# Kernel tuning notes

Hardware: AMD Instinct MI355X
Metric: run time of the kernel (lower is better)

The kernel has to match this reference:

```python
import jax, jax.numpy as jnp
import numpy as np

EMBED_DIM = 768
NUM_HEADS = 12
HEAD_DIM = EMBED_DIM // NUM_HEADS


def setup_inputs() -> dict:
    key = jax.random.key(0)
    k_x, k_wqkv, k_bqkv, k_wp, k_bp = jax.random.split(key, 5)
    B, S, D = 4, 2048, EMBED_DIM
    # nn.Linear default init scale ~ 1/sqrt(fan_in); exact distribution irrelevant for a reference
    lim = 1.0 / np.sqrt(D)
    x = jax.random.normal(k_x, (B, S, D), dtype=jnp.float32)
    w_qkv = jax.random.uniform(k_wqkv, (D, 3 * D), jnp.float32, -lim, lim)
    b_qkv = jax.random.uniform(k_bqkv, (3 * D,), jnp.float32, -lim, lim)
    w_proj = jax.random.uniform(k_wp, (D, D), jnp.float32, -lim, lim)
    b_proj = jax.random.uniform(k_bp, (D,), jnp.float32, -lim, lim)
    return {"x": x, "w_qkv": w_qkv, "b_qkv": b_qkv, "w_proj": w_proj, "b_proj": b_proj}


def reference(x, w_qkv, b_qkv, w_proj, b_proj):
    B, S, D = x.shape
    H, Hd = NUM_HEADS, HEAD_DIM
    qkv = x @ w_qkv + b_qkv                      # [B,S,3D]
    qkv = qkv.reshape(B, S, 3, H, Hd)
    qkv = jnp.transpose(qkv, (2, 0, 3, 1, 4))     # [3,B,H,S,Hd]
    q, k, v = qkv[0], qkv[1], qkv[2]
    scale = 1.0 / np.sqrt(Hd).astype(np.float32)
    scores = jnp.einsum("bhsd,bhtd->bhst", q, k) * scale  # [B,H,S,S]
    attn = jax.nn.softmax(scores, axis=-1)
    out = jnp.einsum("bhst,bhtd->bhsd", attn, v)  # [B,H,S,Hd]
    out = jnp.transpose(out, (0, 2, 1, 3)).reshape(B, S, D)
    return out @ w_proj + b_proj
```

## Files before the change

### kernel.cpp

```cpp
#include <hip/hip_runtime.h>


typedef _Float16 f16;
typedef _Float16 f16x8 __attribute__((ext_vector_type(8)));
typedef _Float16 f16x4 __attribute__((ext_vector_type(4)));
typedef float f32x4 __attribute__((ext_vector_type(4)));

#define BQ 4
#define SQ 2048
#define DQ 768
#define HQ 12
#define HD 64
#define M_TOK (BQ*SQ)
#define KVB 64
#define QSCALE 0.18033688f
#define THR_LOG2 11.5f

__device__ __forceinline__ void gld_lds16(const f16* g, f16* l) {
  __builtin_amdgcn_global_load_lds((const __attribute__((address_space(1))) void*)g,
                                   (__attribute__((address_space(3))) void*)l,
                                   16, 0, 0);
}

__global__ __launch_bounds__(256)
void prep(const float* __restrict__ x, f16* __restrict__ xh,
          const float* __restrict__ w_qkv, f16* __restrict__ wqkvT,
          const float* __restrict__ w_proj, f16* __restrict__ wprojT)
{
  __shared__ float tile[32][33];
  const int bid = blockIdx.x, tid = threadIdx.x;
  if (bid < 6144) {
    int i = (bid * 256 + tid) * 4;
    float4 v = *(const float4*)(x + i);
    f16x4 o = { (f16)v.x, (f16)v.y, (f16)v.z, (f16)v.w };
    *(f16x4*)(xh + i) = o;
    return;
  }
  const float* w; f16* wt; int K, N, nb, kb;
  if (bid < 7872) {
    int b2 = bid - 6144; w = w_qkv; wt = wqkvT; K = DQ; N = 3 * DQ;
    nb = (b2 % 72) * 32; kb = (b2 / 72) * 32;
  } else {
    int b3 = bid - 7872; w = w_proj; wt = wprojT; K = DQ; N = DQ;
    nb = (b3 % 24) * 32; kb = (b3 / 24) * 32;
  }
  int tx = tid & 31, ty = tid >> 5;
  for (int r = ty; r < 32; r += 8)
    tile[r][tx] = w[(size_t)(kb + r) * N + nb + tx];
  __syncthreads();
  for (int r = ty; r < 32; r += 8)
    wt[(size_t)(nb + r) * K + kb + tx] = (f16)tile[tx][r];
}

template<int MODE>
__global__ __launch_bounds__(256, 2)
void gemm128(const f16* __restrict__ A, const f16* __restrict__ Bt,
             const float* __restrict__ bias, float* __restrict__ Cf,
             f16* __restrict__ Qb, f16* __restrict__ Kb, f16* __restrict__ Vt,
             int M, int N, int K, int nbx)
{
  __shared__ f16 Ash[2][128 * 32];
  __shared__ f16 Bsh[2][128 * 32];
  const int tid = threadIdx.x;
  const int bid = blockIdx.x;
  const int nb = bid % nbx, mb = bid / nbx;
  const int m0 = mb * 128, n0 = nb * 128;
  const int lane = tid & 63, wid = tid >> 6;
  const int wr = wid >> 1, wc = wid & 1;
  const int l16 = lane & 15, l4 = lane >> 4;

  f32x4 acc[4][4] = {};

  const int f0 = tid, f1 = tid + 256;
  const f16* a0 = A + (size_t)(m0 + (f0 >> 2)) * K + (f0 & 3) * 8;
  const f16* a1 = A + (size_t)(m0 + (f1 >> 2)) * K + (f1 & 3) * 8;
  const f16* b0 = Bt + (size_t)(n0 + (f0 >> 2)) * K + (f0 & 3) * 8;
  const f16* b1 = Bt + (size_t)(n0 + (f1 >> 2)) * K + (f1 & 3) * 8;

#define GSTAGE(buf, k0)                                   \
  do {                                                    \
    gld_lds16(a0 + (k0), Ash[buf] + f0 * 8);              \
    gld_lds16(a1 + (k0), Ash[buf] + f1 * 8);              \
    gld_lds16(b0 + (k0), Bsh[buf] + f0 * 8);              \
    gld_lds16(b1 + (k0), Bsh[buf] + f1 * 8);              \
  } while (0)

  GSTAGE(0, 0);
  __syncthreads();
  for (int k0 = 0; k0 < K; k0 += 32) {
    const int buf = (k0 >> 5) & 1;
    if (k0 + 32 < K) GSTAGE(buf ^ 1, k0 + 32);
    f16x8 af[4], bfr[4];
    #pragma unroll
    for (int m = 0; m < 4; ++m)
      af[m] = *(const f16x8*)(Ash[buf] + (wr * 64 + m * 16 + l16) * 32 + l4 * 8);
    #pragma unroll
    for (int n = 0; n < 4; ++n)
      bfr[n] = *(const f16x8*)(Bsh[buf] + (wc * 64 + n * 16 + l16) * 32 + l4 * 8);
    #pragma unroll
    for (int m = 0; m < 4; ++m)
      #pragma unroll
      for (int n = 0; n < 4; ++n)
        acc[m][n] = __builtin_amdgcn_mfma_f32_16x16x32_f16(af[m], bfr[n], acc[m][n], 0, 0, 0);
    __syncthreads();
  }
#undef GSTAGE

  const int cbase = n0 + wc * 64;
  const int rbase = m0 + wr * 64;
  if (MODE == 1) {
    #pragma unroll
    for (int n = 0; n < 4; ++n) {
      int c = cbase + n * 16 + l16;
      float bv = bias[c];
      #pragma unroll
      for (int m = 0; m < 4; ++m)
        #pragma unroll
        for (int r = 0; r < 4; ++r) {
          int rr = rbase + m * 16 + l4 * 4 + r;
          Cf[(size_t)rr * N + c] = acc[m][n][r] + bv;
        }
    }
  } else {
    #pragma unroll
    for (int n = 0; n < 4; ++n) {
      int c = cbase + n * 16 + l16;
      float bv = bias[c];
      int which = c / DQ;
      int rem = c - which * DQ;
      int h = rem >> 6, hd = rem & 63;
      #pragma unroll
      for (int m = 0; m < 4; ++m) {
        int rr0 = rbase + m * 16 + l4 * 4;
        int b = rr0 >> 11, s = rr0 & 2047;
        size_t bh = (size_t)(b * HQ + h);
        if (which == 2) {
          f16x4 ov = { (f16)(acc[m][n][0] + bv), (f16)(acc[m][n][1] + bv),
                       (f16)(acc[m][n][2] + bv), (f16)(acc[m][n][3] + bv) };
          *(f16x4*)(Vt + (bh * HD + hd) * SQ + s) = ov;
        } else if (which == 0) {
          #pragma unroll
          for (int r = 0; r < 4; ++r)
            Qb[(bh * SQ + s + r) * HD + hd] = (f16)((acc[m][n][r] + bv) * QSCALE);
        } else {
          #pragma unroll
          for (int r = 0; r < 4; ++r)
            Kb[(bh * SQ + s + r) * HD + hd] = (f16)(acc[m][n][r] + bv);
        }
      }
    }
  }
}

__device__ __forceinline__ int permK(int p) {
  return ((p & 16) << 1) | (((p >> 2) & 3) << 3) | ((p & 32) >> 3) | (p & 3);
}

__global__ __launch_bounds__(256, 3)
void attn(const f16* __restrict__ Qb, const f16* __restrict__ Kb,
          const f16* __restrict__ Vt, f16* __restrict__ O)
{
  __shared__ f16 Ksh[2][KVB * HD];
  __shared__ f16 Vsh[2][HD * KVB];
  const int tid = threadIdx.x, lane = tid & 63, wid = tid >> 6;
  const int l16 = lane & 15, l4 = lane >> 4;

  const int nwg = gridDim.x;
  const int cpx = nwg >> 3;
  const int swz = (blockIdx.x & 7) * cpx + (blockIdx.x >> 3);
  const int qt = swz & 15, bh = swz >> 4;
  const int b = bh / HQ, h = bh - b * HQ;
  const f16* q  = Qb + (size_t)bh * SQ * HD;
  const f16* kp = Kb + (size_t)bh * SQ * HD;
  const f16* vp = Vt + (size_t)bh * HD * SQ;
  const int s0 = qt * 128 + wid * 32;

  f16x8 qf[2][2];
  #pragma unroll
  for (int g = 0; g < 2; ++g)
    #pragma unroll
    for (int kk = 0; kk < 2; ++kk)
      qf[g][kk] = *(const f16x8*)(q + (size_t)(s0 + g * 16 + l16) * HD + kk * 32 + l4 * 8);

  f32x4 oacc[2][4] = {};
  float mrun[2] = { -1e30f, -1e30f }, lrun[2] = { 0.f, 0.f };

  const int p0 = tid >> 3, p1 = (tid >> 3) + 32;
  const int scS = ((tid & 7) ^ (p0 & 7)) * 8;
  const int kr0 = permK(p0), kr1 = permK(p1);

#define STAGE(buf, t0)                                                        \
  do {                                                                        \
    gld_lds16(kp + (size_t)((t0) + kr0) * HD + scS, Ksh[buf] + tid * 8);      \
    gld_lds16(kp + (size_t)((t0) + kr1) * HD + scS, Ksh[buf] + (tid + 256) * 8);\
    gld_lds16(vp + (size_t)p0 * SQ + (t0) + scS,   Vsh[buf] + tid * 8);       \
    gld_lds16(vp + (size_t)p1 * SQ + (t0) + scS,   Vsh[buf] + (tid + 256) * 8);\
  } while (0)

#define COMPUTE(buf)                                                          \
  do {                                                                        \
    f32x4 sacc[2][4] = {};                                                    \
    __builtin_amdgcn_s_setprio(1);                                            \
    _Pragma("unroll")                                                         \
    for (int kk = 0; kk < 2; ++kk) {                                          \
      f16x8 kf[4];                                                            \
      _Pragma("unroll")                                                       \
      for (int n = 0; n < 4; ++n)                                             \
        kf[n] = *(const f16x8*)(Ksh[buf] + (n * 16 + l16) * HD +              \
                                ((kk * 32 + l4 * 8) ^ ((l16 & 7) * 8)));      \
      _Pragma("unroll")                                                       \
      for (int n = 0; n < 4; ++n) {                                           \
        sacc[0][n] = __builtin_amdgcn_mfma_f32_16x16x32_f16(kf[n], qf[0][kk], sacc[0][n], 0, 0, 0); \
        sacc[1][n] = __builtin_amdgcn_mfma_f32_16x16x32_f16(kf[n], qf[1][kk], sacc[1][n], 0, 0, 0); \
      }                                                                       \
    }                                                                         \
    __builtin_amdgcn_s_setprio(0);                                            \
    f16x8 bfr[2][2];                                                          \
    _Pragma("unroll")                                                         \
    for (int g = 0; g < 2; ++g) {                                             \
      float rm = -1e30f;                                                      \
      _Pragma("unroll")                                                       \
      for (int n = 0; n < 4; ++n)                                             \
        rm = fmaxf(rm, fmaxf(fmaxf(sacc[g][n][0], sacc[g][n][1]),             \
                             fmaxf(sacc[g][n][2], sacc[g][n][3])));           \
      rm = fmaxf(rm, __shfl_xor(rm, 16));                                     \
      rm = fmaxf(rm, __shfl_xor(rm, 32));                                     \
      if (!__all(rm - mrun[g] <= THR_LOG2)) {                                 \
        float mn = fmaxf(mrun[g], rm);                                        \
        float corr = __builtin_amdgcn_exp2f(mrun[g] - mn);                    \
        lrun[g] *= corr;                                                      \
        _Pragma("unroll")                                                     \
        for (int n = 0; n < 4; ++n)                                           \
          oacc[g][n] *= corr;                                                 \
        mrun[g] = mn;                                                         \
      }                                                                       \
      float mref = mrun[g];                                                   \
      float ps = 0.f;                                                         \
      _Pragma("unroll")                                                       \
      for (int n = 0; n < 4; ++n)                                             \
        _Pragma("unroll")                                                     \
        for (int r = 0; r < 4; ++r) {                                         \
          float pv = __builtin_amdgcn_exp2f(sacc[g][n][r] - mref);            \
          bfr[g][n & 1][(n >> 1) * 4 + r] = (f16)pv;                          \
          ps += pv;                                                           \
        }                                                                     \
      ps += __shfl_xor(ps, 16);                                               \
      ps += __shfl_xor(ps, 32);                                               \
      lrun[g] += ps;                                                          \
    }                                                                         \
    __builtin_amdgcn_s_setprio(1);                                            \
    _Pragma("unroll")                                                         \
    for (int kk = 0; kk < 2; ++kk) {                                          \
      f16x8 vf[4];                                                            \
      _Pragma("unroll")                                                       \
      for (int n = 0; n < 4; ++n)                                             \
        vf[n] = *(const f16x8*)(Vsh[buf] + (n * 16 + l16) * KVB +             \
                                ((kk * 32 + l4 * 8) ^ ((l16 & 7) * 8)));      \
      _Pragma("unroll")                                                       \
      for (int n = 0; n < 4; ++n) {                                           \
        oacc[0][n] = __builtin_amdgcn_mfma_f32_16x16x32_f16(vf[n], bfr[0][kk], oacc[0][n], 0, 0, 0); \
        oacc[1][n] = __builtin_amdgcn_mfma_f32_16x16x32_f16(vf[n], bfr[1][kk], oacc[1][n], 0, 0, 0); \
      }                                                                       \
    }                                                                         \
    __builtin_amdgcn_s_setprio(0);                                            \
  } while (0)

  STAGE(0, 0);
  __syncthreads();
  for (int t0 = 0; t0 < SQ; t0 += 2 * KVB) {
    STAGE(1, t0 + KVB);
    COMPUTE(0);
    __syncthreads();
    if (t0 + 2 * KVB < SQ) STAGE(0, t0 + 2 * KVB);
    COMPUTE(1);
    __syncthreads();
  }
#undef STAGE
#undef COMPUTE

  #pragma unroll
  for (int g = 0; g < 2; ++g) {
    float inv = 1.f / lrun[g];
    const int s = s0 + g * 16 + l16;
    f16* obase = O + ((size_t)b * SQ + s) * DQ + h * HD + l4 * 4;
    #pragma unroll
    for (int n = 0; n < 4; ++n) {
      f16x4 ov = { (f16)(oacc[g][n][0] * inv), (f16)(oacc[g][n][1] * inv),
                   (f16)(oacc[g][n][2] * inv), (f16)(oacc[g][n][3] * inv) };
      *(f16x4*)(obase + n * 16) = ov;
    }
  }
}

extern "C" void kernel_launch(void* const* d_in, const int* in_sizes, int n_in,
                              void* d_out, int out_size, void* d_ws, size_t ws_size,
                              hipStream_t stream) {
  const float* x      = (const float*)d_in[0];
  const float* w_qkv  = (const float*)d_in[1];
  const float* b_qkv  = (const float*)d_in[2];
  const float* w_proj = (const float*)d_in[3];
  const float* b_proj = (const float*)d_in[4];
  float* out = (float*)d_out;

  char* ws = (char*)d_ws;
  f16* xh     = (f16*)ws; ws += (size_t)M_TOK * DQ * 2;
  f16* wqkvT  = (f16*)ws; ws += (size_t)3 * DQ * DQ * 2;
  f16* wprojT = (f16*)ws; ws += (size_t)DQ * DQ * 2;
  f16* Qb     = (f16*)ws; ws += (size_t)M_TOK * DQ * 2;
  f16* Kb     = (f16*)ws; ws += (size_t)M_TOK * DQ * 2;
  f16* Vt     = (f16*)ws; ws += (size_t)M_TOK * DQ * 2;
  f16* AO     = xh;

  prep<<<8448, 256, 0, stream>>>(x, xh, w_qkv, wqkvT, w_proj, wprojT);

  gemm128<0><<<(M_TOK / 128) * (3 * DQ / 128), 256, 0, stream>>>(
      xh, wqkvT, b_qkv, nullptr, Qb, Kb, Vt, M_TOK, 3 * DQ, DQ, 3 * DQ / 128);

  attn<<<BQ * HQ * (SQ / 128), 256, 0, stream>>>(Qb, Kb, Vt, AO);

  gemm128<1><<<(M_TOK / 128) * (DQ / 128), 256, 0, stream>>>(
      AO, wprojT, b_proj, out, nullptr, nullptr, nullptr, M_TOK, DQ, DQ, DQ / 128);
}
```

Before: 164.6 us.

## Software-pipeline attention loop: overlap next QK^T with softmax and PV

Restructures the flash-attention inner loop so the QK^T MFMAs for tile t+1 are issued before the softmax and PV of tile t, using two score register sets. K and V loads are now staged separately and one tile apart, so V for a tile arrives while its scores are being computed. The aim is to hide the exp/reduction latency of softmax behind matrix-core work from the next tile. The cost is an extra 32 floats of score registers per lane, which may lower occupancy or cause spills.

```diff
diff --git a/kernel.cpp b/kernel.cpp
--- a/kernel.cpp
+++ b/kernel.cpp
@@ -13,6 +13,7 @@
 #define HD 64
 #define M_TOK (BQ*SQ)
 #define KVB 64
+#define NT (SQ/KVB)
 #define QSCALE 0.18033688f
 #define THR_LOG2 11.5f
 
@@ -189,94 +190,120 @@
   const int scS = ((tid & 7) ^ (p0 & 7)) * 8;
   const int kr0 = permK(p0), kr1 = permK(p1);
 
-#define STAGE(buf, t0)                                                        \
-  do {                                                                        \
-    gld_lds16(kp + (size_t)((t0) + kr0) * HD + scS, Ksh[buf] + tid * 8);      \
-    gld_lds16(kp + (size_t)((t0) + kr1) * HD + scS, Ksh[buf] + (tid + 256) * 8);\
-    gld_lds16(vp + (size_t)p0 * SQ + (t0) + scS,   Vsh[buf] + tid * 8);       \
-    gld_lds16(vp + (size_t)p1 * SQ + (t0) + scS,   Vsh[buf] + (tid + 256) * 8);\
+#define STAGE_K(buf, toff)                                                     \
+  do {                                                                         \
+    gld_lds16(kp + (size_t)((toff) + kr0) * HD + scS, Ksh[buf] + tid * 8);     \
+    gld_lds16(kp + (size_t)((toff) + kr1) * HD + scS, Ksh[buf] + (tid + 256) * 8);\
   } while (0)
-
-#define COMPUTE(buf)                                                          \
-  do {                                                                        \
-    f32x4 sacc[2][4] = {};                                                    \
-    __builtin_amdgcn_s_setprio(1);                                            \
-    _Pragma("unroll")                                                         \
-    for (int kk = 0; kk < 2; ++kk) {                                          \
-      f16x8 kf[4];                                                            \
-      _Pragma("unroll")                                                       \
-      for (int n = 0; n < 4; ++n)                                             \
-        kf[n] = *(const f16x8*)(Ksh[buf] + (n * 16 + l16) * HD +              \
-                                ((kk * 32 + l4 * 8) ^ ((l16 & 7) * 8)));      \
-      _Pragma("unroll")                                                       \
-      for (int n = 0; n < 4; ++n) {                                           \
-        sacc[0][n] = __builtin_amdgcn_mfma_f32_16x16x32_f16(kf[n], qf[0][kk], sacc[0][n], 0, 0, 0); \
-        sacc[1][n] = __builtin_amdgcn_mfma_f32_16x16x32_f16(kf[n], qf[1][kk], sacc[1][n], 0, 0, 0); \
-      }                                                                       \
-    }                                                                         \
-    __builtin_amdgcn_s_setprio(0);                                            \
-    f16x8 bfr[2][2];                                                          \
-    _Pragma("unroll")                                                         \
-    for (int g = 0; g < 2; ++g) {                                             \
-      float rm = -1e30f;                                                      \
-      _Pragma("unroll")                                                       \
-      for (int n = 0; n < 4; ++n)                                             \
-        rm = fmaxf(rm, fmaxf(fmaxf(sacc[g][n][0], sacc[g][n][1]),             \
-                             fmaxf(sacc[g][n][2], sacc[g][n][3])));           \
-      rm = fmaxf(rm, __shfl_xor(rm, 16));                                     \
-      rm = fmaxf(rm, __shfl_xor(rm, 32));                                     \
-      if (!__all(rm - mrun[g] <= THR_LOG2)) {                                 \
-        float mn = fmaxf(mrun[g], rm);                                        \
-        float corr = __builtin_amdgcn_exp2f(mrun[g] - mn);                    \
-        lrun[g] *= corr;                                                      \
-        _Pragma("unroll")                                                     \
-        for (int n = 0; n < 4; ++n)                                           \
-          oacc[g][n] *= corr;                                                 \
-        mrun[g] = mn;                                                         \
-      }                                                                       \
-      float mref = mrun[g];                                                   \
-      float ps = 0.f;                                                         \
-      _Pragma("unroll")                                                       \
-      for (int n = 0; n < 4; ++n)                                             \
-        _Pragma("unroll")                                                     \
-        for (int r = 0; r < 4; ++r) {                                         \
-          float pv = __builtin_amdgcn_exp2f(sacc[g][n][r] - mref);            \
-          bfr[g][n & 1][(n >> 1) * 4 + r] = (f16)pv;                          \
-          ps += pv;                                                           \
-        }                                                                     \
-      ps += __shfl_xor(ps, 16);                                               \
-      ps += __shfl_xor(ps, 32);                                               \
-      lrun[g] += ps;                                                          \
-    }                                                                         \
-    __builtin_amdgcn_s_setprio(1);                                            \
-    _Pragma("unroll")                                                         \
-    for (int kk = 0; kk < 2; ++kk) {                                          \
-      f16x8 vf[4];                                                            \
-      _Pragma("unroll")                                                       \
-      for (int n = 0; n < 4; ++n)                                             \
-        vf[n] = *(const f16x8*)(Vsh[buf] + (n * 16 + l16) * KVB +             \
-                                ((kk * 32 + l4 * 8) ^ ((l16 & 7) * 8)));      \
-      _Pragma("unroll")                                                       \
-      for (int n = 0; n < 4; ++n) {                                           \
-        oacc[0][n] = __builtin_amdgcn_mfma_f32_16x16x32_f16(vf[n], bfr[0][kk], oacc[0][n], 0, 0, 0); \
-        oacc[1][n] = __builtin_amdgcn_mfma_f32_16x16x32_f16(vf[n], bfr[1][kk], oacc[1][n], 0, 0, 0); \
-      }                                                                       \
-    }                                                                         \
-    __builtin_amdgcn_s_setprio(0);                                            \
+#define STAGE_V(buf, toff)                                                     \
+  do {                                                                         \
+    gld_lds16(vp + (size_t)p0 * SQ + (toff) + scS, Vsh[buf] + tid * 8);        \
+    gld_lds16(vp + (size_t)p1 * SQ + (toff) + scS, Vsh[buf] + (tid + 256) * 8);\
   } while (0)
 
-  STAGE(0, 0);
+  auto QKT = [&](f32x4 (&S)[2][4], int kbuf) {
+    #pragma unroll
+    for (int g = 0; g < 2; ++g)
+      #pragma unroll
+      for (int n = 0; n < 4; ++n)
+        S[g][n] = (f32x4){0.f, 0.f, 0.f, 0.f};
+    const f16* Kbase = Ksh[kbuf];
+    __builtin_amdgcn_s_setprio(1);
+    #pragma unroll
+    for (int kk = 0; kk < 2; ++kk) {
+      f16x8 kf[4];
+      #pragma unroll
+      for (int n = 0; n < 4; ++n)
+        kf[n] = *(const f16x8*)(Kbase + (n * 16 + l16) * HD +
+                                ((kk * 32 + l4 * 8) ^ ((l16 & 7) * 8)));
+      #pragma unroll
+      for (int n = 0; n < 4; ++n) {
+        S[0][n] = __builtin_amdgcn_mfma_f32_16x16x32_f16(kf[n], qf[0][kk], S[0][n], 0, 0, 0);
+        S[1][n] = __builtin_amdgcn_mfma_f32_16x16x32_f16(kf[n], qf[1][kk], S[1][n], 0, 0, 0);
+      }
+    }
+    __builtin_amdgcn_s_setprio(0);
+  };
+
+  auto SMPV = [&](f32x4 (&S)[2][4], int vbuf) {
+    f16x8 bfr[2][2];
+    #pragma unroll
+    for (int g = 0; g < 2; ++g) {
+      float rm = -1e30f;
+      #pragma unroll
+      for (int n = 0; n < 4; ++n)
+        rm = fmaxf(rm, fmaxf(fmaxf(S[g][n][0], S[g][n][1]),
+                             fmaxf(S[g][n][2], S[g][n][3])));
+      rm = fmaxf(rm, __shfl_xor(rm, 16));
+      rm = fmaxf(rm, __shfl_xor(rm, 32));
+      if (!__all(rm - mrun[g] <= THR_LOG2)) {
+        float mn = fmaxf(mrun[g], rm);
+        float corr = __builtin_amdgcn_exp2f(mrun[g] - mn);
+        lrun[g] *= corr;
+        #pragma unroll
+        for (int n = 0; n < 4; ++n)
+          oacc[g][n] *= corr;
+        mrun[g] = mn;
+      }
+      float mref = mrun[g];
+      float ps = 0.f;
+      #pragma unroll
+      for (int n = 0; n < 4; ++n)
+        #pragma unroll
+        for (int r = 0; r < 4; ++r) {
+          float pv = __builtin_amdgcn_exp2f(S[g][n][r] - mref);
+          bfr[g][n & 1][(n >> 1) * 4 + r] = (f16)pv;
+          ps += pv;
+        }
+      ps += __shfl_xor(ps, 16);
+      ps += __shfl_xor(ps, 32);
+      lrun[g] += ps;
+    }
+    const f16* Vbase = Vsh[vbuf];
+    __builtin_amdgcn_s_setprio(1);
+    #pragma unroll
+    for (int kk = 0; kk < 2; ++kk) {
+      f16x8 vf[4];
+      #pragma unroll
+      for (int n = 0; n < 4; ++n)
+        vf[n] = *(const f16x8*)(Vbase + (n * 16 + l16) * KVB +
+                                ((kk * 32 + l4 * 8) ^ ((l16 & 7) * 8)));
+      #pragma unroll
+      for (int n = 0; n < 4; ++n) {
+        oacc[0][n] = __builtin_amdgcn_mfma_f32_16x16x32_f16(vf[n], bfr[0][kk], oacc[0][n], 0, 0, 0);
+        oacc[1][n] = __builtin_amdgcn_mfma_f32_16x16x32_f16(vf[n], bfr[1][kk], oacc[1][n], 0, 0, 0);
+      }
+    }
+    __builtin_amdgcn_s_setprio(0);
+  };
+
+  f32x4 sA[2][4], sB[2][4];
+
+  STAGE_K(0, 0);
   __syncthreads();
-  for (int t0 = 0; t0 < SQ; t0 += 2 * KVB) {
-    STAGE(1, t0 + KVB);
-    COMPUTE(0);
+  STAGE_K(1, KVB);
+  STAGE_V(0, 0);
+  QKT(sA, 0);
+  __syncthreads();
+
+  for (int t = 1; t < NT; t += 2) {
+    if (t + 1 < NT) STAGE_K((t + 1) & 1, (t + 1) * KVB);
+    STAGE_V(t & 1, t * KVB);
+    QKT(sB, t & 1);
+    SMPV(sA, (t - 1) & 1);
     __syncthreads();
-    if (t0 + 2 * KVB < SQ) STAGE(0, t0 + 2 * KVB);
-    COMPUTE(1);
-    __syncthreads();
-  }
-#undef STAGE
-#undef COMPUTE
+    if (t + 1 < NT) {
+      if (t + 2 < NT) STAGE_K((t + 2) & 1, (t + 2) * KVB);
+      STAGE_V((t + 1) & 1, (t + 1) * KVB);
+      QKT(sA, (t + 1) & 1);
+      SMPV(sB, t & 1);
+      __syncthreads();
+    }
+  }
+  SMPV(sB, (NT - 1) & 1);
+
+#undef STAGE_K
+#undef STAGE_V
 
   #pragma unroll
   for (int g = 0; g < 2; ++g) {
```

Result: no change. 165.8 us (+0.7%).

## Double GEMM K-tile to 64 with XOR-swizzled LDS layout

Applied to the files above, without the earlier changes.

Each GEMM main-loop iteration now processes a K-slice of 64 instead of 32, halving the number of barriers and loop iterations. The LDS layout for the A and B tiles is XOR-swizzled on 16-byte chunks so that fragment reads across rows avoid bank conflicts. The cost is LDS use doubling to 64KB per block, which may limit two-blocks-per-CU occupancy.

```diff
diff --git a/kernel.cpp b/kernel.cpp
--- a/kernel.cpp
+++ b/kernel.cpp
@@ -59,8 +59,8 @@
              f16* __restrict__ Qb, f16* __restrict__ Kb, f16* __restrict__ Vt,
              int M, int N, int K, int nbx)
 {
-  __shared__ f16 Ash[2][128 * 32];
-  __shared__ f16 Bsh[2][128 * 32];
+  __shared__ f16 Ash[2][128 * 64];
+  __shared__ f16 Bsh[2][128 * 64];
   const int tid = threadIdx.x;
   const int bid = blockIdx.x;
   const int nb = bid % nbx, mb = bid / nbx;
@@ -71,37 +71,50 @@
 
   f32x4 acc[4][4] = {};
 
-  const int f0 = tid, f1 = tid + 256;
-  const f16* a0 = A + (size_t)(m0 + (f0 >> 2)) * K + (f0 & 3) * 8;
-  const f16* a1 = A + (size_t)(m0 + (f1 >> 2)) * K + (f1 & 3) * 8;
-  const f16* b0 = Bt + (size_t)(n0 + (f0 >> 2)) * K + (f0 & 3) * 8;
-  const f16* b1 = Bt + (size_t)(n0 + (f1 >> 2)) * K + (f1 & 3) * 8;
+  const f16* aP[4]; const f16* bP[4]; int lOff[4];
+  #pragma unroll
+  for (int j = 0; j < 4; ++j) {
+    int q = j * 256 + tid;
+    int r = q >> 3;
+    int sc = ((q & 7) ^ (r & 7)) * 8;
+    aP[j] = A  + (size_t)(m0 + r) * K + sc;
+    bP[j] = Bt + (size_t)(n0 + r) * K + sc;
+    lOff[j] = q * 8;
+  }
 
 #define GSTAGE(buf, k0)                                   \
   do {                                                    \
-    gld_lds16(a0 + (k0), Ash[buf] + f0 * 8);              \
-    gld_lds16(a1 + (k0), Ash[buf] + f1 * 8);              \
-    gld_lds16(b0 + (k0), Bsh[buf] + f0 * 8);              \
-    gld_lds16(b1 + (k0), Bsh[buf] + f1 * 8);              \
+    _Pragma("unroll")                                     \
+    for (int j = 0; j < 4; ++j) {                         \
+      gld_lds16(aP[j] + (k0), Ash[buf] + lOff[j]);        \
+      gld_lds16(bP[j] + (k0), Bsh[buf] + lOff[j]);        \
+    }                                                     \
   } while (0)
 
   GSTAGE(0, 0);
   __syncthreads();
-  for (int k0 = 0; k0 < K; k0 += 32) {
-    const int buf = (k0 >> 5) & 1;
-    if (k0 + 32 < K) GSTAGE(buf ^ 1, k0 + 32);
-    f16x8 af[4], bfr[4];
-    #pragma unroll
-    for (int m = 0; m < 4; ++m)
-      af[m] = *(const f16x8*)(Ash[buf] + (wr * 64 + m * 16 + l16) * 32 + l4 * 8);
-    #pragma unroll
-    for (int n = 0; n < 4; ++n)
-      bfr[n] = *(const f16x8*)(Bsh[buf] + (wc * 64 + n * 16 + l16) * 32 + l4 * 8);
-    #pragma unroll
-    for (int m = 0; m < 4; ++m)
-      #pragma unroll
-      for (int n = 0; n < 4; ++n)
-        acc[m][n] = __builtin_amdgcn_mfma_f32_16x16x32_f16(af[m], bfr[n], acc[m][n], 0, 0, 0);
+  for (int k0 = 0; k0 < K; k0 += 64) {
+    const int buf = (k0 >> 6) & 1;
+    if (k0 + 64 < K) GSTAGE(buf ^ 1, k0 + 64);
+    #pragma unroll
+    for (int kk = 0; kk < 2; ++kk) {
+      f16x8 af[4], bfr[4];
+      #pragma unroll
+      for (int m = 0; m < 4; ++m) {
+        int R = wr * 64 + m * 16 + l16;
+        af[m] = *(const f16x8*)(Ash[buf] + R * 64 + (((kk * 4 + l4) ^ (R & 7)) * 8));
+      }
+      #pragma unroll
+      for (int n = 0; n < 4; ++n) {
+        int R = wc * 64 + n * 16 + l16;
+        bfr[n] = *(const f16x8*)(Bsh[buf] + R * 64 + (((kk * 4 + l4) ^ (R & 7)) * 8));
+      }
+      #pragma unroll
+      for (int m = 0; m < 4; ++m)
+        #pragma unroll
+        for (int n = 0; n < 4; ++n)
+          acc[m][n] = __builtin_amdgcn_mfma_f32_16x16x32_f16(af[m], bfr[n], acc[m][n], 0, 0, 0);
+    }
     __syncthreads();
   }
 #undef GSTAGE
```

Measured after the change: 160.0 us. -2.8%, faster.
